# Performance work log

Measured on AMD Instinct MI355X. Metric: run time of the kernel, lower is better.

The kernel has to match this reference:

```python
import jax, jax.numpy as jnp
import numpy as np

DIM, H, W, DEPTH = 256, 64, 64, 4
D_STATE, DT_RANK, D_CONV = 8, 16, 4
G, AGENTS = 8, 4

PKEYS = ['ln_w','ln_b','in_proj_w','conv_w','conv_b','x_proj_w','dt_proj_w','dt_proj_b',
         'A_log','A_b_log','D','out_proj_w','mn_w','mn_b']


def layernorm(x, w, b, eps=1e-5):
    mu = jnp.mean(x, -1, keepdims=True)
    var = jnp.var(x, -1, keepdims=True)
    return (x - mu) * jax.lax.rsqrt(var + eps) * w + b


def causal_conv1d(x, w, b):
    # x: (g, d, L); w: (d, k) depthwise causal conv (pad left k-1)
    k = w.shape[-1]
    xp = jnp.pad(x, ((0, 0), (0, 0), (k - 1, 0)))
    y = jax.lax.conv_general_dilated(xp, w[:, None, :], (1,), 'VALID',
                                     dimension_numbers=('NCH', 'OIH', 'NCH'),
                                     feature_group_count=w.shape[0])
    return y + b[None, :, None]


def selective_scan(u, delta, A, B, C, Dp, z):
    # u, delta, z: (g, d, L); B, C: (g, n, L); A: (d, n); Dp: (d,)
    dT = jnp.moveaxis(delta, -1, 0)
    BT = jnp.moveaxis(B, -1, 0)
    CT = jnp.moveaxis(C, -1, 0)
    uT = jnp.moveaxis(u, -1, 0)
    h0 = jnp.zeros(u.shape[:2] + (A.shape[-1],), u.dtype)  # (g, d, n)

    def step(h, inp):
        d_t, B_t, C_t, u_t = inp  # (g,d),(g,n),(g,n),(g,d)
        h = jnp.exp(d_t[..., None] * A) * h + (d_t * u_t)[..., None] * B_t[:, None, :]
        return h, jnp.einsum('gdn,gn->gd', h, C_t)

    _, ys = jax.lax.scan(step, h0, (dT, BT, CT, uT))
    y = jnp.moveaxis(ys, 0, -1) + Dp[None, :, None] * u
    return y * jax.nn.silu(z)


def ssm_dir(xdl, zdl, p, A):
    # one scan direction of mamba_inner_fn_no_out_proj; xdl, zdl: (g, d, L)
    xc = jax.nn.silu(causal_conv1d(xdl, p['conv_w'], p['conv_b']))
    x_dbl = jnp.einsum('gdl,ed->gel', xc, p['x_proj_w'])  # e = dt_rank + 2n
    dt, B, C = jnp.split(x_dbl, [DT_RANK, DT_RANK + D_STATE], axis=1)
    delta = jax.nn.softplus(jnp.einsum('grl,dr->gdl', dt, p['dt_proj_w'])
                            + p['dt_proj_b'][None, :, None])
    return selective_scan(xc, delta, A, B, C, p['D'], zdl)


def single_mamba_block(x, p):
    # x: (g, L, c)  -- LayerNorm + bidirectional Mamba (bimamba v1) + residual
    skip = x
    xn = layernorm(x, p['ln_w'], p['ln_b'])
    xz = jnp.einsum('glc,ec->gle', xn, p['in_proj_w'])  # (g, L, 2d), no bias
    xx, z = jnp.split(xz, 2, axis=-1)
    xdl = jnp.swapaxes(xx, 1, 2)
    zdl = jnp.swapaxes(z, 1, 2)
    y_f = ssm_dir(xdl, zdl, p, -jnp.exp(p['A_log']))
    y_b = jnp.flip(ssm_dir(jnp.flip(xdl, -1), jnp.flip(zdl, -1), p, -jnp.exp(p['A_b_log'])), -1)
    y = 0.5 * (y_f + y_b)  # if_devide_out=True
    out = jnp.einsum('gdl,od->glo', y, p['out_proj_w'])  # no bias
    out = layernorm(out, p['mn_w'], p['mn_b'])  # use_norm=True
    return out + skip


def _forward(data, plist, record_len):
    b, c, h, w = data.shape
    rl = np.asarray(record_len)
    seg = jnp.asarray(np.repeat(np.arange(rl.shape[0]), rl))
    means = jax.ops.segment_sum(data, seg, num_segments=rl.shape[0]) \
        / jnp.asarray(rl, data.dtype)[:, None, None, None]
    x = means.reshape(rl.shape[0], c, h * w).transpose(0, 2, 1)  # (G, L, C)
    for i in range(DEPTH):
        p = {k: v[i] for k, v in zip(PKEYS, plist)}
        x = single_mamba_block(x, p)
    return x.transpose(0, 2, 1).reshape(rl.shape[0], c, h, w)


def setup_inputs() -> dict:
    key = jax.random.key(0)
    ks = jax.random.split(key, 8)
    nrm = lambda k, shape, sc: jax.random.normal(k, shape, jnp.float32) * sc
    Alog = jnp.zeros((DEPTH, DIM, D_STATE), jnp.float32) \
        + jnp.log(jnp.arange(1, D_STATE + 1, dtype=jnp.float32))
    return {
        'data': jax.random.normal(ks[0], (G * AGENTS, DIM, H, W), jnp.float32),
        'ln_w': jnp.ones((DEPTH, DIM)), 'ln_b': jnp.zeros((DEPTH, DIM)),
        'in_proj_w': nrm(ks[1], (DEPTH, 2 * DIM, DIM), 0.02),
        'conv_w': nrm(ks[2], (DEPTH, DIM, D_CONV), 0.3),
        'conv_b': jnp.zeros((DEPTH, DIM)),
        'x_proj_w': nrm(ks[3], (DEPTH, DT_RANK + 2 * D_STATE, DIM), 0.02),
        'dt_proj_w': nrm(ks[4], (DEPTH, DIM, DT_RANK), 0.1),
        'dt_proj_b': jnp.full((DEPTH, DIM), float(np.log(np.expm1(0.01))), jnp.float32),
        'A_log': Alog, 'A_b_log': Alog,
        'D': jnp.ones((DEPTH, DIM)),
        'out_proj_w': nrm(ks[5], (DEPTH, DIM, DIM), 0.02),
        'mn_w': jnp.ones((DEPTH, DIM)), 'mn_b': jnp.zeros((DEPTH, DIM)),
        'record_len': jnp.full((G,), AGENTS, dtype=jnp.int32),
    }


def reference(data, ln_w, ln_b, in_proj_w, conv_w, conv_b, x_proj_w, dt_proj_w, dt_proj_b,
              A_log, A_b_log, D, out_proj_w, mn_w, mn_b, record_len):
    plist = [ln_w, ln_b, in_proj_w, conv_w, conv_b, x_proj_w, dt_proj_w, dt_proj_b,
             A_log, A_b_log, D, out_proj_w, mn_w, mn_b]
    return _forward(data, plist, record_len)
```

## Files before the change

### kernel.cpp

```cpp
#include <hip/hip_runtime.h>
#include <hip/hip_bf16.h>
#include <cstdint>
#include <cstddef>

typedef unsigned short u16;
typedef unsigned int   u32;

typedef short s16x8 __attribute__((ext_vector_type(8)));
typedef float f32x4 __attribute__((ext_vector_type(4)));

__device__ __forceinline__ float b2f(u16 u){ u32 x = ((u32)u)<<16; float f; __builtin_memcpy(&f,&x,4); return f; }
__device__ __forceinline__ u16  f2b(float f){ u32 x; __builtin_memcpy(&x,&f,4); u32 r = x + 0x7FFFu + ((x>>16)&1u); return (u16)(r>>16); }

__device__ __forceinline__ void unpack8(uint4 v, float* o){
  o[0]=b2f((u16)v.x); o[1]=b2f((u16)(v.x>>16));
  o[2]=b2f((u16)v.y); o[3]=b2f((u16)(v.y>>16));
  o[4]=b2f((u16)v.z); o[5]=b2f((u16)(v.z>>16));
  o[6]=b2f((u16)v.w); o[7]=b2f((u16)(v.w>>16));
}

__device__ __forceinline__ void gl_lds16(const u16* g, u16* l){
  __builtin_amdgcn_global_load_lds((const __attribute__((address_space(1))) u32*)g,
                                   (__attribute__((address_space(3))) u32*)l, 16, 0, 0);
}

__global__ void k_detect(const u16* __restrict__ lnw, int* __restrict__ flag){
  if (threadIdx.x==0 && blockIdx.x==0) *flag = (lnw[0] == 0x3F80) ? 1 : 0;
}

struct CvtTable { const void* src[14]; u16* dst[14]; int n[14]; };
__global__ void k_cvt(CvtTable t, const int* __restrict__ flag){
  int ti = blockIdx.y;
  int n = t.n[ti];
  int isbf = *flag;
  const u16*  sb = (const u16*)t.src[ti];
  const float* sf = (const float*)t.src[ti];
  u16* d = t.dst[ti];
  for (int i = blockIdx.x*256 + threadIdx.x; i < n; i += gridDim.x*256)
    d[i] = isbf ? sb[i] : f2b(sf[i]);
}

__global__ void k_mean(const void* __restrict__ data, const int* __restrict__ rl,
                       float* __restrict__ x, const int* __restrict__ flag){
  __shared__ float tile[32][129];
  int isbf = *flag;
  const u16*  db = (const u16*)data;
  const float* df_ = (const float*)data;
  int g = blockIdx.z, c0 = blockIdx.y*32, l0 = blockIdx.x*128;
  int tid = threadIdx.x;
  int off=0; for(int i=0;i<g;i++) off += rl[i];
  int cnt = rl[g];
  float inv = 1.0f/(float)cnt;
  for(int it=0; it<16; ++it){
    int idx = it*256 + tid;
    int ci = idx>>7, lj = idx&127;
    float acc = 0.f;
    for(int b=0;b<cnt;b++){
      size_t gi = ((size_t)(off+b)*256 + (c0+ci)) * 4096 + (l0+lj);
      acc += isbf ? b2f(db[gi]) : df_[gi];
    }
    tile[ci][lj] = acc*inv;
  }
  __syncthreads();
  for(int it=0; it<16; ++it){
    int idx = it*256 + tid;
    int lj = idx>>5, ci = idx&31;
    x[ ((size_t)g*4096 + (l0+lj))*256 + (c0+ci) ] = tile[ci][lj];
  }
}

__global__ void k_prep(const u16* __restrict__ dtp, const u16* __restrict__ xpw, u16* __restrict__ bcomb){
  int layer = blockIdx.y, row = blockIdx.x, c = threadIdx.x;
  u16 out;
  if (row < 256){
    float acc = 0.f;
    #pragma unroll
    for(int r=0;r<16;r++)
      acc += b2f(dtp[(size_t)layer*4096 + row*16 + r]) * b2f(xpw[(size_t)layer*8192 + r*256 + c]);
    out = f2b(acc);
  } else if (row < 272){
    out = xpw[(size_t)layer*8192 + (16 + row - 256)*256 + c];
  } else {
    out = 0;
  }
  bcomb[((size_t)layer*384 + row)*256 + c] = out;
}

__global__ void k_ln1(const float* __restrict__ x, u16* __restrict__ xn,
                      const u16* __restrict__ w, const u16* __restrict__ b, int layer){
  int wid = threadIdx.x>>6, lane = threadIdx.x&63;
  int row = blockIdx.x*4 + wid;
  const float* xr = x + (size_t)row*256;
  float4 v = *(const float4*)(xr + lane*4);
  float s = v.x+v.y+v.z+v.w;
  float q = v.x*v.x+v.y*v.y+v.z*v.z+v.w*v.w;
  for(int o=32;o;o>>=1){ s += __shfl_xor(s,o); q += __shfl_xor(q,o); }
  float mu = s*(1.f/256.f);
  float var = q*(1.f/256.f) - mu*mu;
  float rs = rsqrtf(var + 1e-5f);
  const u16* wp = w + layer*256 + lane*4;
  const u16* bp = b + layer*256 + lane*4;
  float vv[4] = {v.x,v.y,v.z,v.w};
  u16 o4[4];
  #pragma unroll
  for(int k2=0;k2<4;k2++) o4[k2] = f2b( (vv[k2]-mu)*rs*b2f(wp[k2]) + b2f(bp[k2]) );
  uint2 ov; ov.x = (u32)o4[0] | ((u32)o4[1]<<16); ov.y = (u32)o4[2] | ((u32)o4[3]<<16);
  *(uint2*)(xn + (size_t)row*256 + lane*4) = ov;
}

template<int MODE>
__global__ __launch_bounds__(256)
void k_gemm(const u16* __restrict__ A, const u16* __restrict__ B,
            u16* __restrict__ C0, int ldC,
            const u16* __restrict__ bias, u16* __restrict__ C1){
  __shared__ u16 As[128*64];
  __shared__ u16 Bs[128*64];
  int tid = threadIdx.x, wid = tid>>6, lane = tid&63;
  int m0 = blockIdx.x*128, n0 = blockIdx.y*128;
  f32x4 acc[4][4];
  #pragma unroll
  for(int i=0;i<4;i++)
    #pragma unroll
    for(int j=0;j<4;j++) acc[i][j] = (f32x4){0.f,0.f,0.f,0.f};
  int lrow  = lane>>3;
  int scol  = ((lane&7) ^ lrow) * 8;
  int rm = (wid&1)*64, cn = (wid>>1)*64;
  for(int k0=0;k0<256;k0+=64){
    #pragma unroll
    for(int it=0; it<4; ++it){
      int chunk = wid*4 + it;
      int row = chunk*8 + lrow;
      gl_lds16(A + (size_t)(m0+row)*256 + k0 + scol, As + chunk*512 + lane*8);
      gl_lds16(B + (size_t)(n0+row)*256 + k0 + scol, Bs + chunk*512 + lane*8);
    }
    __syncthreads();
    #pragma unroll
    for(int kk=0;kk<2;kk++){
      s16x8 af[4], bfr[4];
      #pragma unroll
      for(int i=0;i<4;i++){
        int ar = rm + i*16 + (lane&15);
        int ap = (kk*4 + (lane>>4)) ^ (ar&7);
        af[i]  = *(const s16x8*)(As + ar*64 + ap*8);
        int br = cn + i*16 + (lane&15);
        int bp = (kk*4 + (lane>>4)) ^ (br&7);
        bfr[i] = *(const s16x8*)(Bs + br*64 + bp*8);
      }
      #pragma unroll
      for(int i=0;i<4;i++)
        #pragma unroll
        for(int j=0;j<4;j++)
          acc[i][j] = __builtin_amdgcn_mfma_f32_16x16x32_bf16(af[i], bfr[j], acc[i][j], 0,0,0);
    }
    __syncthreads();
  }
  #pragma unroll
  for(int i=0;i<4;i++){
    #pragma unroll
    for(int j=0;j<4;j++){
      int n  = n0 + cn + j*16 + (lane&15);
      int mB = m0 + rm + i*16 + ((lane>>4)<<2);
      #pragma unroll
      for(int r=0;r<4;r++){
        float val = acc[i][j][r];
        int m = mB + r;
        if (MODE==0){
          C0[(size_t)m*ldC + n] = f2b(val);
        } else {
          if (n < 256){
            float v2 = val + b2f(bias[n]);
            float sp = (v2 > 15.f) ? v2 : __logf(1.f + __expf(v2));
            C0[(size_t)m*256 + n] = f2b(sp);
          } else if (n < 272){
            C1[(size_t)m*16 + (n-256)] = f2b(val);
          }
        }
      }
    }
  }
}

__global__ void k_conv(const u16* __restrict__ xz, const u16* __restrict__ cw,
                       const u16* __restrict__ cb, u16* __restrict__ xcf, u16* __restrict__ xcb_, int layer){
  int l0 = blockIdx.x*4, g = blockIdx.y, d = threadIdx.x;
  float w[4];
  #pragma unroll
  for(int j=0;j<4;j++) w[j] = b2f(cw[(size_t)layer*1024 + d*4 + j]);
  float bb = b2f(cb[layer*256 + d]);
  float xv[10];
  #pragma unroll
  for(int t=0;t<10;t++){
    int lp = l0 - 3 + t;
    xv[t] = (lp>=0 && lp<4096) ? b2f(xz[((size_t)g*4096 + lp)*512 + d]) : 0.f;
  }
  #pragma unroll
  for(int i=0;i<4;i++){
    float af = bb, ab = bb;
    #pragma unroll
    for(int j=0;j<4;j++){ af += w[j]*xv[i+j]; ab += w[j]*xv[i+6-j]; }
    af = af / (1.f + __expf(-af));
    ab = ab / (1.f + __expf(-ab));
    size_t o = ((size_t)g*4096 + (l0+i))*256 + d;
    xcf[o]  = f2b(af);
    xcb_[o] = f2b(ab);
  }
}

__global__ __launch_bounds__(256)
void k_scan1(const u16* __restrict__ df, const u16* __restrict__ db,
             const u16* __restrict__ uf, const u16* __restrict__ ub,
             const u16* __restrict__ bcf, const u16* __restrict__ bcb,
             const u16* __restrict__ Alog, const u16* __restrict__ Ablog,
             float* __restrict__ abuf, float* __restrict__ bbuf, int layer){
  int c = blockIdx.x, g = blockIdx.y, dir = blockIdx.z, d = threadIdx.x;
  const u16* dl = dir ? db : df;
  const u16* uu = dir ? ub : uf;
  const u16* bc = dir ? bcb : bcf;
  const u16* Al = dir ? Ablog : Alog;
  float An[8], h[8], ap[8];
  #pragma unroll
  for(int n=0;n<8;n++){
    An[n] = -__expf(b2f(Al[(size_t)layer*2048 + d*8 + n]));
    h[n] = 0.f; ap[n] = 1.f;
  }
  #pragma unroll 4
  for(int t=0;t<64;t++){
    int ts = c*64 + t;
    int tg = dir ? (4095 - ts) : ts;
    size_t rowo = (size_t)g*4096 + tg;
    float dv = b2f(dl[rowo*256 + d]);
    float uv = b2f(uu[rowo*256 + d]);
    uint4 bv = *(const uint4*)(bc + rowo*16);
    float bn[8]; unpack8(bv, bn);
    float du = dv*uv;
    #pragma unroll
    for(int n=0;n<8;n++){
      float da = __expf(dv*An[n]);
      h[n] = fmaf(da, h[n], du*bn[n]);
      ap[n] *= da;
    }
  }
  size_t base = ((((size_t)dir*8+g)*64 + c)*256 + d)*8;
  *(float4*)(abuf+base)   = (float4){ap[0],ap[1],ap[2],ap[3]};
  *(float4*)(abuf+base+4) = (float4){ap[4],ap[5],ap[6],ap[7]};
  *(float4*)(bbuf+base)   = (float4){h[0],h[1],h[2],h[3]};
  *(float4*)(bbuf+base+4) = (float4){h[4],h[5],h[6],h[7]};
}

__global__ void k_scan2(const float* __restrict__ abuf, const float* __restrict__ bbuf,
                        float* __restrict__ hs){
  int dblk = blockIdx.x, g = blockIdx.y, dir = blockIdx.z;
  int n = threadIdx.x & 7, dd = threadIdx.x >> 3;
  int d = dblk*32 + dd;
  float h = 0.f;
  size_t gofs = (((size_t)dir*8+g)*64);
  for(int c=0;c<64;c++){
    size_t idx = ((gofs + c)*256 + d)*8 + n;
    hs[idx] = h;
    h = fmaf(abuf[idx], h, bbuf[idx]);
  }
}

#define AP 264
template<int LAST>
__global__ __launch_bounds__(256)
void k_scanout(const u16* __restrict__ df, const u16* __restrict__ db,
               const u16* __restrict__ uf, const u16* __restrict__ ub,
               const u16* __restrict__ bcf, const u16* __restrict__ bcb,
               const u16* __restrict__ Alog, const u16* __restrict__ Ablog,
               const u16* __restrict__ Dp, const u16* __restrict__ xz,
               const float* __restrict__ hs,
               const u16* __restrict__ Bw,
               float* __restrict__ X, u16* __restrict__ xn_next,
               const u16* __restrict__ mnw, const u16* __restrict__ mnb,
               const u16* __restrict__ lnw_n, const u16* __restrict__ lnb_n,
               int layer){
  __shared__ u16 As[64*AP];
  __shared__ u16 Bs[256*64];
  int tid = threadIdx.x;
  int c = blockIdx.x, g = blockIdx.y;
  int l0 = c*64;
  int d = tid;
  float Dd = b2f(Dp[layer*256 + d]);
  float An[8], h[8];
  {
    #pragma unroll
    for(int n=0;n<8;n++) An[n] = -__expf(b2f(Ablog[(size_t)layer*2048 + d*8 + n]));
    size_t base = ((((size_t)8+g)*64 + (63-c))*256 + d)*8;
    float4 h0 = *(const float4*)(hs+base);
    float4 h1 = *(const float4*)(hs+base+4);
    h[0]=h0.x; h[1]=h0.y; h[2]=h0.z; h[3]=h0.w;
    h[4]=h1.x; h[5]=h1.y; h[6]=h1.z; h[7]=h1.w;
    #pragma unroll 2
    for(int q=0;q<64;q++){
      int t = 63 - q;
      size_t rowo = (size_t)g*4096 + l0 + t;
      float dv = b2f(db[rowo*256 + d]);
      float uv = b2f(ub[rowo*256 + d]);
      uint4 bv = *(const uint4*)(bcb + rowo*16);
      uint4 cv = *(const uint4*)(bcb + rowo*16 + 8);
      float bn[8], cn_[8];
      unpack8(bv, bn); unpack8(cv, cn_);
      float du = dv*uv;
      float y = 0.f;
      #pragma unroll
      for(int n=0;n<8;n++){
        float da = __expf(dv*An[n]);
        h[n] = fmaf(da, h[n], du*bn[n]);
        y = fmaf(h[n], cn_[n], y);
      }
      y += Dd*uv;
      float zv = b2f(xz[rowo*512 + 256 + d]);
      y *= 0.5f * zv / (1.f + __expf(-zv));
      As[t*AP + d] = f2b(y);
    }
  }
  {
    #pragma unroll
    for(int n=0;n<8;n++) An[n] = -__expf(b2f(Alog[(size_t)layer*2048 + d*8 + n]));
    size_t base = (((size_t)g*64 + c)*256 + d)*8;
    float4 h0 = *(const float4*)(hs+base);
    float4 h1 = *(const float4*)(hs+base+4);
    h[0]=h0.x; h[1]=h0.y; h[2]=h0.z; h[3]=h0.w;
    h[4]=h1.x; h[5]=h1.y; h[6]=h1.z; h[7]=h1.w;
    #pragma unroll 2
    for(int t=0;t<64;t++){
      size_t rowo = (size_t)g*4096 + l0 + t;
      float dv = b2f(df[rowo*256 + d]);
      float uv = b2f(uf[rowo*256 + d]);
      uint4 bv = *(const uint4*)(bcf + rowo*16);
      uint4 cv = *(const uint4*)(bcf + rowo*16 + 8);
      float bn[8], cn_[8];
      unpack8(bv, bn); unpack8(cv, cn_);
      float du = dv*uv;
      float y = 0.f;
      #pragma unroll
      for(int n=0;n<8;n++){
        float da = __expf(dv*An[n]);
        h[n] = fmaf(da, h[n], du*bn[n]);
        y = fmaf(h[n], cn_[n], y);
      }
      y += Dd*uv;
      float zv = b2f(xz[rowo*512 + 256 + d]);
      y *= 0.5f * zv / (1.f + __expf(-zv));
      int off = t*AP + d;
      As[off] = f2b(b2f(As[off]) + y);
    }
  }
  int wid = tid>>6, lane = tid&63;
  f32x4 acc[16];
  #pragma unroll
  for(int j=0;j<16;j++) acc[j] = (f32x4){0.f,0.f,0.f,0.f};
  int lrow = lane>>3;
  int scol = ((lane&7) ^ lrow) * 8;
  for(int k0=0;k0<256;k0+=64){
    #pragma unroll
    for(int it=0; it<8; ++it){
      int chunk = wid*8 + it;
      int row = chunk*8 + lrow;
      gl_lds16(Bw + (size_t)row*256 + k0 + scol, Bs + chunk*512 + lane*8);
    }
    __syncthreads();
    #pragma unroll
    for(int kk=0;kk<2;kk++){
      int ar = wid*16 + (lane&15);
      s16x8 af = *(const s16x8*)(As + ar*AP + k0 + kk*32 + (lane>>4)*8);
      #pragma unroll
      for(int j=0;j<16;j++){
        int br = j*16 + (lane&15);
        int bp = (kk*4 + (lane>>4)) ^ (br&7);
        s16x8 bf = *(const s16x8*)(Bs + br*64 + bp*8);
        acc[j] = __builtin_amdgcn_mfma_f32_16x16x32_bf16(af, bf, acc[j], 0,0,0);
      }
    }
    __syncthreads();
  }
  size_t gm0 = (size_t)g*4096 + l0;
  int quad = lane>>4;
  float sm[4]={0,0,0,0}, sq[4]={0,0,0,0};
  #pragma unroll
  for(int j=0;j<16;j++)
    #pragma unroll
    for(int r=0;r<4;r++){ float v=acc[j][r]; sm[r]+=v; sq[r]+=v*v; }
  #pragma unroll
  for(int o=1;o<16;o<<=1)
    #pragma unroll
    for(int r=0;r<4;r++){ sm[r]+=__shfl_xor(sm[r],o); sq[r]+=__shfl_xor(sq[r],o); }
  float mu[4], rs[4];
  #pragma unroll
  for(int r=0;r<4;r++){
    mu[r] = sm[r]*(1.f/256.f);
    float var = sq[r]*(1.f/256.f) - mu[r]*mu[r];
    rs[r] = rsqrtf(var + 1e-5f);
  }
  #pragma unroll
  for(int j=0;j<16;j++){
    int col = j*16 + (lane&15);
    float w = b2f(mnw[col]), bb = b2f(mnb[col]);
    #pragma unroll
    for(int r=0;r<4;r++){
      size_t m = gm0 + wid*16 + quad*4 + r;
      float xn = X[m*256 + col] + (acc[j][r]-mu[r])*rs[r]*w + bb;
      X[m*256 + col] = xn;
      acc[j][r] = xn;
    }
  }
  if (!LAST){
    float sm2[4]={0,0,0,0}, sq2[4]={0,0,0,0};
    #pragma unroll
    for(int j=0;j<16;j++)
      #pragma unroll
      for(int r=0;r<4;r++){ float v=acc[j][r]; sm2[r]+=v; sq2[r]+=v*v; }
    #pragma unroll
    for(int o=1;o<16;o<<=1)
      #pragma unroll
      for(int r=0;r<4;r++){ sm2[r]+=__shfl_xor(sm2[r],o); sq2[r]+=__shfl_xor(sq2[r],o); }
    float mu2[4], rs2[4];
    #pragma unroll
    for(int r=0;r<4;r++){
      mu2[r] = sm2[r]*(1.f/256.f);
      float var = sq2[r]*(1.f/256.f) - mu2[r]*mu2[r];
      rs2[r] = rsqrtf(var + 1e-5f);
    }
    #pragma unroll
    for(int j=0;j<16;j++){
      int col = j*16 + (lane&15);
      float w = b2f(lnw_n[col]), bb = b2f(lnb_n[col]);
      #pragma unroll
      for(int r=0;r<4;r++){
        size_t m = gm0 + wid*16 + quad*4 + r;
        xn_next[m*256 + col] = f2b((acc[j][r]-mu2[r])*rs2[r]*w + bb);
      }
    }
  }
}

__global__ void k_tr(const float* __restrict__ x, void* __restrict__ out, const int* __restrict__ flag){
  __shared__ float tile[32][129];
  int isbf = *flag;
  int l0 = blockIdx.x*128, c0 = blockIdx.y*32, g = blockIdx.z;
  int tid = threadIdx.x;
  for(int it=0; it<16; ++it){
    int idx = it*256 + tid;
    int lj = idx>>5, ci = idx&31;
    tile[ci][lj] = x[((size_t)g*4096 + l0+lj)*256 + c0+ci];
  }
  __syncthreads();
  for(int it=0; it<16; ++it){
    int idx = it*256 + tid;
    int lj = idx&127, ci = idx>>7;
    size_t o = ((size_t)g*256 + c0+ci)*4096 + l0+lj;
    float v = tile[ci][lj];
    if (isbf) ((u16*)out)[o] = f2b(v);
    else      ((float*)out)[o] = v;
  }
}

extern "C" void kernel_launch(void* const* d_in, const int* in_sizes, int n_in,
                              void* d_out, int out_size, void* d_ws, size_t ws_size,
                              hipStream_t stream){
  (void)in_sizes; (void)n_in; (void)out_size; (void)ws_size;
  const int* rl = (const int*)d_in[15];

  char* ws = (char*)d_ws;
  float* X    = (float*)(ws);
  u16*  XN    = (u16*)(ws + 33554432);
  u16*  XZ    = (u16*)(ws + 50331648);
  u16*  XCF   = (u16*)(ws + 83886080);
  u16*  XCB   = (u16*)(ws + 100663296);
  u16*  DF    = (u16*)(ws + 117440512);
  u16*  DB    = (u16*)(ws + 134217728);
  u16*  BCF   = (u16*)(ws + 150994944);
  u16*  BCB   = (u16*)(ws + 152043520);
  u16*  BCOMB = (u16*)(ws + 153092096);
  float* ABUF = (float*)(ws + 153878528);
  float* BBUF = (float*)(ws + 162267136);
  float* HS   = (float*)(ws + 170655744);
  u16*  WCVT  = (u16*)(ws + 195821568);
  int*  FLAG  = (int*)(ws + 197918720);

  u16* W_lnw  = WCVT + 0;
  u16* W_lnb  = WCVT + 1024;
  u16* W_inp  = WCVT + 2048;
  u16* W_cw   = WCVT + 526336;
  u16* W_cb   = WCVT + 530432;
  u16* W_xp   = WCVT + 531456;
  u16* W_dtw  = WCVT + 564224;
  u16* W_dtb  = WCVT + 580608;
  u16* W_Al   = WCVT + 581632;
  u16* W_Abl  = WCVT + 589824;
  u16* W_D    = WCVT + 598016;
  u16* W_outp = WCVT + 599040;
  u16* W_mnw  = WCVT + 861184;
  u16* W_mnb  = WCVT + 862208;

  k_detect<<<1,64,0,stream>>>((const u16*)d_in[1], FLAG);

  CvtTable t;
  const int idxs[14] = {1,2,3,4,5,6,7,8,9,10,11,12,13,14};
  u16* dsts[14] = {W_lnw,W_lnb,W_inp,W_cw,W_cb,W_xp,W_dtw,W_dtb,W_Al,W_Abl,W_D,W_outp,W_mnw,W_mnb};
  const int ns[14] = {1024,1024,524288,4096,1024,32768,16384,1024,8192,8192,1024,262144,1024,1024};
  for(int i=0;i<14;i++){ t.src[i]=d_in[idxs[i]]; t.dst[i]=dsts[i]; t.n[i]=ns[i]; }
  k_cvt<<<dim3(32,14),256,0,stream>>>(t, FLAG);

  k_mean<<<dim3(32,8,8),256,0,stream>>>(d_in[0], rl, X, FLAG);
  k_prep<<<dim3(384,4),256,0,stream>>>(W_dtw, W_xp, BCOMB);
  k_ln1<<<8192,256,0,stream>>>(X, XN, W_lnw, W_lnb, 0);

  for(int layer=0; layer<4; ++layer){
    k_gemm<0><<<dim3(256,4),256,0,stream>>>(XN, W_inp + (size_t)layer*512*256, XZ, 512, nullptr, nullptr);
    k_conv<<<dim3(1024,8),256,0,stream>>>(XZ, W_cw, W_cb, XCF, XCB, layer);
    k_gemm<1><<<dim3(512,3),256,0,stream>>>(XCF, BCOMB + (size_t)layer*384*256, DF, 256, W_dtb + layer*256, BCF);
    k_scan1<<<dim3(64,8,2),256,0,stream>>>(DF,DB,XCF,XCB,BCF,BCB,W_Al,W_Abl,ABUF,BBUF,layer);
    k_scan2<<<dim3(8,8,2),256,0,stream>>>(ABUF,BBUF,HS);
    if (layer < 3){
      k_scanout<0><<<dim3(64,8),256,0,stream>>>(DF,DB,XCF,XCB,BCF,BCB,W_Al,W_Abl,W_D,XZ,HS,
                                                W_outp + (size_t)layer*256*256, X, XN,
                                                W_mnw + layer*256, W_mnb + layer*256,
                                                W_lnw + (layer+1)*256, W_lnb + (layer+1)*256, layer);
    } else {
      k_scanout<1><<<dim3(64,8),256,0,stream>>>(DF,DB,XCF,XCB,BCF,BCB,W_Al,W_Abl,W_D,XZ,HS,
                                                W_outp + (size_t)layer*256*256, X, XN,
                                                W_mnw + layer*256, W_mnb + layer*256,
                                                W_lnw, W_lnb, layer);
    }
  }
  k_tr<<<dim3(32,8,8),256,0,stream>>>(X, d_out, FLAG);
}
```

Before: 1.135 ms.

## Run forward and backward scans concurrently in scanout with 512-thread blocks

Result: no change. 1.143 ms (+0.7%).

```diff
diff --git a/kernel.cpp b/kernel.cpp
--- a/kernel.cpp
+++ b/kernel.cpp
@@ -263,7 +263,7 @@
 
 #define AP 264
 template<int LAST>
-__global__ __launch_bounds__(256)
+__global__ __launch_bounds__(512, 4)
 void k_scanout(const u16* __restrict__ df, const u16* __restrict__ db,
                const u16* __restrict__ uf, const u16* __restrict__ ub,
                const u16* __restrict__ bcf, const u16* __restrict__ bcb,
@@ -277,28 +277,34 @@
                int layer){
   __shared__ u16 As[64*AP];
   __shared__ u16 Bs[256*64];
+  __shared__ float redm[8][4][4], redq[8][4][4];
   int tid = threadIdx.x;
   int c = blockIdx.x, g = blockIdx.y;
   int l0 = c*64;
-  int d = tid;
-  float Dd = b2f(Dp[layer*256 + d]);
-  float An[8], h[8];
   {
-    #pragma unroll
-    for(int n=0;n<8;n++) An[n] = -__expf(b2f(Ablog[(size_t)layer*2048 + d*8 + n]));
-    size_t base = ((((size_t)8+g)*64 + (63-c))*256 + d)*8;
+    int dir = tid >> 8;
+    int d = tid & 255;
+    const u16* dl = dir ? db : df;
+    const u16* uu = dir ? ub : uf;
+    const u16* bc = dir ? bcb : bcf;
+    const u16* Al = dir ? Ablog : Alog;
+    float Dd = b2f(Dp[layer*256 + d]);
+    float An[8], h[8];
+    #pragma unroll
+    for(int n=0;n<8;n++) An[n] = -__expf(b2f(Al[(size_t)layer*2048 + d*8 + n]));
+    size_t base = ((((size_t)dir*8+g)*64 + (dir ? (63-c) : c))*256 + d)*8;
     float4 h0 = *(const float4*)(hs+base);
     float4 h1 = *(const float4*)(hs+base+4);
     h[0]=h0.x; h[1]=h0.y; h[2]=h0.z; h[3]=h0.w;
     h[4]=h1.x; h[5]=h1.y; h[6]=h1.z; h[7]=h1.w;
     #pragma unroll 2
     for(int q=0;q<64;q++){
-      int t = 63 - q;
+      int t = dir ? (63-q) : q;
       size_t rowo = (size_t)g*4096 + l0 + t;
-      float dv = b2f(db[rowo*256 + d]);
-      float uv = b2f(ub[rowo*256 + d]);
-      uint4 bv = *(const uint4*)(bcb + rowo*16);
-      uint4 cv = *(const uint4*)(bcb + rowo*16 + 8);
+      float dv = b2f(dl[rowo*256 + d]);
+      float uv = b2f(uu[rowo*256 + d]);
+      uint4 bv = *(const uint4*)(bc + rowo*16);
+      uint4 cv = *(const uint4*)(bc + rowo*16 + 8);
       float bn[8], cn_[8];
       unpack8(bv, bn); unpack8(cv, cn_);
       float du = dv*uv;
@@ -312,63 +318,55 @@
       y += Dd*uv;
       float zv = b2f(xz[rowo*512 + 256 + d]);
       y *= 0.5f * zv / (1.f + __expf(-zv));
-      As[t*AP + d] = f2b(y);
-    }
-  }
+      if (dir) Bs[t*256 + d] = f2b(y);
+      else     As[t*AP  + d] = f2b(y);
+    }
+  }
+  __syncthreads();
   {
-    #pragma unroll
-    for(int n=0;n<8;n++) An[n] = -__expf(b2f(Alog[(size_t)layer*2048 + d*8 + n]));
-    size_t base = (((size_t)g*64 + c)*256 + d)*8;
-    float4 h0 = *(const float4*)(hs+base);
-    float4 h1 = *(const float4*)(hs+base+4);
-    h[0]=h0.x; h[1]=h0.y; h[2]=h0.z; h[3]=h0.w;
-    h[4]=h1.x; h[5]=h1.y; h[6]=h1.z; h[7]=h1.w;
-    #pragma unroll 2
-    for(int t=0;t<64;t++){
-      size_t rowo = (size_t)g*4096 + l0 + t;
-      float dv = b2f(df[rowo*256 + d]);
-      float uv = b2f(uf[rowo*256 + d]);
-      uint4 bv = *(const uint4*)(bcf + rowo*16);
-      uint4 cv = *(const uint4*)(bcf + rowo*16 + 8);
-      float bn[8], cn_[8];
-      unpack8(bv, bn); unpack8(cv, cn_);
-      float du = dv*uv;
-      float y = 0.f;
-      #pragma unroll
-      for(int n=0;n<8;n++){
-        float da = __expf(dv*An[n]);
-        h[n] = fmaf(da, h[n], du*bn[n]);
-        y = fmaf(h[n], cn_[n], y);
+    int row = tid >> 3, seg = tid & 7;
+    u16* pa = As + row*AP + seg*32;
+    const u16* pb = Bs + row*256 + seg*32;
+    #pragma unroll
+    for(int k2=0;k2<4;k2++){
+      uint4 a = *(const uint4*)(pa + k2*8);
+      uint4 b = *(const uint4*)(pb + k2*8);
+      float fa[8], fb[8]; unpack8(a,fa); unpack8(b,fb);
+      u32 o[4];
+      #pragma unroll
+      for(int j=0;j<4;j++){
+        u16 lo = f2b(fa[2*j]  +fb[2*j]);
+        u16 hi = f2b(fa[2*j+1]+fb[2*j+1]);
+        o[j] = (u32)lo | ((u32)hi<<16);
       }
-      y += Dd*uv;
-      float zv = b2f(xz[rowo*512 + 256 + d]);
-      y *= 0.5f * zv / (1.f + __expf(-zv));
-      int off = t*AP + d;
-      As[off] = f2b(b2f(As[off]) + y);
-    }
-  }
+      *(uint4*)(pa + k2*8) = (uint4){o[0],o[1],o[2],o[3]};
+    }
+  }
+  __syncthreads();
   int wid = tid>>6, lane = tid&63;
-  f32x4 acc[16];
-  #pragma unroll
-  for(int j=0;j<16;j++) acc[j] = (f32x4){0.f,0.f,0.f,0.f};
+  int mb = wid & 3, nh = wid >> 2;
+  f32x4 acc[8];
+  #pragma unroll
+  for(int j=0;j<8;j++) acc[j] = (f32x4){0.f,0.f,0.f,0.f};
   int lrow = lane>>3;
   int scol = ((lane&7) ^ lrow) * 8;
+  int quad = lane>>4;
   for(int k0=0;k0<256;k0+=64){
     #pragma unroll
-    for(int it=0; it<8; ++it){
-      int chunk = wid*8 + it;
+    for(int it=0; it<4; ++it){
+      int chunk = wid*4 + it;
       int row = chunk*8 + lrow;
       gl_lds16(Bw + (size_t)row*256 + k0 + scol, Bs + chunk*512 + lane*8);
     }
     __syncthreads();
     #pragma unroll
     for(int kk=0;kk<2;kk++){
-      int ar = wid*16 + (lane&15);
-      s16x8 af = *(const s16x8*)(As + ar*AP + k0 + kk*32 + (lane>>4)*8);
-      #pragma unroll
-      for(int j=0;j<16;j++){
-        int br = j*16 + (lane&15);
-        int bp = (kk*4 + (lane>>4)) ^ (br&7);
+      int ar = mb*16 + (lane&15);
+      s16x8 af = *(const s16x8*)(As + ar*AP + k0 + kk*32 + quad*8);
+      #pragma unroll
+      for(int j=0;j<8;j++){
+        int br = (nh*8+j)*16 + (lane&15);
+        int bp = (kk*4 + quad) ^ (br&7);
         s16x8 bf = *(const s16x8*)(Bs + br*64 + bp*8);
         acc[j] = __builtin_amdgcn_mfma_f32_16x16x32_bf16(af, bf, acc[j], 0,0,0);
       }
@@ -376,30 +374,36 @@
     __syncthreads();
   }
   size_t gm0 = (size_t)g*4096 + l0;
-  int quad = lane>>4;
   float sm[4]={0,0,0,0}, sq[4]={0,0,0,0};
   #pragma unroll
-  for(int j=0;j<16;j++)
+  for(int j=0;j<8;j++)
     #pragma unroll
     for(int r=0;r<4;r++){ float v=acc[j][r]; sm[r]+=v; sq[r]+=v*v; }
   #pragma unroll
   for(int o=1;o<16;o<<=1)
     #pragma unroll
     for(int r=0;r<4;r++){ sm[r]+=__shfl_xor(sm[r],o); sq[r]+=__shfl_xor(sq[r],o); }
+  if ((lane&15)==0){
+    #pragma unroll
+    for(int r=0;r<4;r++){ redm[wid][quad][r]=sm[r]; redq[wid][quad][r]=sq[r]; }
+  }
+  __syncthreads();
   float mu[4], rs[4];
   #pragma unroll
   for(int r=0;r<4;r++){
-    mu[r] = sm[r]*(1.f/256.f);
-    float var = sq[r]*(1.f/256.f) - mu[r]*mu[r];
+    float smt = redm[wid][quad][r] + redm[wid^4][quad][r];
+    float sqt = redq[wid][quad][r] + redq[wid^4][quad][r];
+    mu[r] = smt*(1.f/256.f);
+    float var = sqt*(1.f/256.f) - mu[r]*mu[r];
     rs[r] = rsqrtf(var + 1e-5f);
   }
   #pragma unroll
-  for(int j=0;j<16;j++){
-    int col = j*16 + (lane&15);
+  for(int j=0;j<8;j++){
+    int col = nh*128 + j*16 + (lane&15);
     float w = b2f(mnw[col]), bb = b2f(mnb[col]);
     #pragma unroll
     for(int r=0;r<4;r++){
-      size_t m = gm0 + wid*16 + quad*4 + r;
+      size_t m = gm0 + mb*16 + quad*4 + r;
       float xn = X[m*256 + col] + (acc[j][r]-mu[r])*rs[r]*w + bb;
       X[m*256 + col] = xn;
       acc[j][r] = xn;
@@ -408,27 +412,35 @@
   if (!LAST){
     float sm2[4]={0,0,0,0}, sq2[4]={0,0,0,0};
     #pragma unroll
-    for(int j=0;j<16;j++)
+    for(int j=0;j<8;j++)
       #pragma unroll
       for(int r=0;r<4;r++){ float v=acc[j][r]; sm2[r]+=v; sq2[r]+=v*v; }
     #pragma unroll
     for(int o=1;o<16;o<<=1)
       #pragma unroll
       for(int r=0;r<4;r++){ sm2[r]+=__shfl_xor(sm2[r],o); sq2[r]+=__shfl_xor(sq2[r],o); }
+    __syncthreads();
+    if ((lane&15)==0){
+      #pragma unroll
+      for(int r=0;r<4;r++){ redm[wid][quad][r]=sm2[r]; redq[wid][quad][r]=sq2[r]; }
+    }
+    __syncthreads();
     float mu2[4], rs2[4];
     #pragma unroll
     for(int r=0;r<4;r++){
-      mu2[r] = sm2[r]*(1.f/256.f);
-      float var = sq2[r]*(1.f/256.f) - mu2[r]*mu2[r];
+      float smt = redm[wid][quad][r] + redm[wid^4][quad][r];
+      float sqt = redq[wid][quad][r] + redq[wid^4][quad][r];
+      mu2[r] = smt*(1.f/256.f);
+      float var = sqt*(1.f/256.f) - mu2[r]*mu2[r];
       rs2[r] = rsqrtf(var + 1e-5f);
     }
     #pragma unroll
-    for(int j=0;j<16;j++){
-      int col = j*16 + (lane&15);
+    for(int j=0;j<8;j++){
+      int col = nh*128 + j*16 + (lane&15);
       float w = b2f(lnw_n[col]), bb = b2f(lnb_n[col]);
       #pragma unroll
       for(int r=0;r<4;r++){
-        size_t m = gm0 + wid*16 + quad*4 + r;
+        size_t m = gm0 + mb*16 + quad*4 + r;
         xn_next[m*256 + col] = f2b((acc[j][r]-mu2[r])*rs2[r]*w + bb);
       }
     }
@@ -514,12 +526,12 @@
     k_scan1<<<dim3(64,8,2),256,0,stream>>>(DF,DB,XCF,XCB,BCF,BCB,W_Al,W_Abl,ABUF,BBUF,layer);
     k_scan2<<<dim3(8,8,2),256,0,stream>>>(ABUF,BBUF,HS);
     if (layer < 3){
-      k_scanout<0><<<dim3(64,8),256,0,stream>>>(DF,DB,XCF,XCB,BCF,BCB,W_Al,W_Abl,W_D,XZ,HS,
+      k_scanout<0><<<dim3(64,8),512,0,stream>>>(DF,DB,XCF,XCB,BCF,BCB,W_Al,W_Abl,W_D,XZ,HS,
                                                 W_outp + (size_t)layer*256*256, X, XN,
                                                 W_mnw + layer*256, W_mnb + layer*256,
                                                 W_lnw + (layer+1)*256, W_lnb + (layer+1)*256, layer);
     } else {
-      k_scanout<1><<<dim3(64,8),256,0,stream>>>(DF,DB,XCF,XCB,BCF,BCB,W_Al,W_Abl,W_D,XZ,HS,
+      k_scanout<1><<<dim3(64,8),512,0,stream>>>(DF,DB,XCF,XCB,BCF,BCB,W_Al,W_Abl,W_D,XZ,HS,
                                                 W_outp + (size_t)layer*256*256, X, XN,
                                                 W_mnw + layer*256, W_mnb + layer*256,
                                                 W_lnw, W_lnb, layer);
```
